# Kernel optimization log

Hardware: AMD Instinct MI355X
Metric: run time of the kernel (lower is better)

Reference implementation:

```python
import jax, jax.numpy as jnp
import numpy as np

U, I, G = 200000, 100000, 10000
D = 64
LAYERS = 3
E_HG = 3_000_000
E_GI = 2_000_000
B = 8192


def setup_inputs() -> dict:
    key = jax.random.key(0)
    ks = jax.random.split(key, 20)
    n_hg = U + G
    n_gi = G + I
    xav = lambda k, shape: (jax.random.normal(k, shape, jnp.float32) * 0.05)
    inp = {
        "user_inputs": jax.random.randint(ks[0], (B,), 0, U),
        "pos_groups": jax.random.randint(ks[1], (B,), 0, G),
        "neg_groups": jax.random.randint(ks[2], (B,), 0, G),
        # hypergraph propagation matrix (normalized-adjacency-like values)
        "hg_rows": jax.random.randint(ks[3], (E_HG,), 0, n_hg),
        "hg_cols": jax.random.randint(ks[4], (E_HG,), 0, n_hg),
        "hg_vals": jax.random.uniform(ks[5], (E_HG,), jnp.float32) / 16.0,
        # group-item bipartite graph (one LightGCN hop)
        "gi_rows": jax.random.randint(ks[6], (E_GI,), 0, n_gi),
        "gi_cols": jax.random.randint(ks[7], (E_GI,), 0, n_gi),
        "gi_vals": jax.random.uniform(ks[8], (E_GI,), jnp.float32) / 16.0,
        # dense group-group overlap matrix
        "gg_graph": jax.random.uniform(ks[9], (G, G), jnp.float32) / float(G),
        # learned parameters
        "user_emb": xav(ks[10], (U, D)),
        "item_emb": xav(ks[11], (I, D)),
        "group_emb": xav(ks[12], (G, D)),
        "hyper_w": xav(ks[13], (D, 1)),
        "hyper_b": jnp.zeros((1,), jnp.float32),
        "lightgcn_w": xav(ks[14], (D, 1)),
        "lightgcn_b": jnp.zeros((1,), jnp.float32),
        "overlap_w": xav(ks[15], (D, 1)),
        "overlap_b": jnp.zeros((1,), jnp.float32),
    }
    return inp


def spmm(rows, cols, vals, x, n):
    # sparse(n,n) @ x : gather cols, scale, scatter-add into rows
    return jax.ops.segment_sum(vals[:, None] * x[cols], rows, num_segments=n)


def reference(user_inputs, pos_groups, neg_groups,
              hg_rows, hg_cols, hg_vals,
              gi_rows, gi_cols, gi_vals,
              gg_graph,
              user_emb, item_emb, group_emb,
              hyper_w, hyper_b, lightgcn_w, lightgcn_b, overlap_w, overlap_b):
    # --- hypergraph branch: layered SpMM + mean over (layers+1) views ---
    hg = jnp.concatenate([user_emb, group_emb], axis=0)  # [U+G, D]
    acc = hg
    cur = hg
    for _ in range(LAYERS):
        cur = spmm(hg_rows, hg_cols, hg_vals, cur, U + G)
        acc = acc + cur
    hg_mean = acc / float(LAYERS + 1)
    hg_users = hg_mean[:U]   # [U, D]
    hg_groups = hg_mean[U:]  # [G, D]

    # --- lightgcn branch: one SpMM hop over group-item graph ---
    gi = jnp.concatenate([group_emb, item_emb], axis=0)  # [G+I, D]
    gi = spmm(gi_rows, gi_cols, gi_vals, gi, G + I)
    gi_groups = gi[:G]

    # --- overlap branch: dense group-group propagation ---
    gg = gg_graph @ group_emb  # [G, D]

    # --- gated multi-view fusion ---
    sig = jax.nn.sigmoid
    hyper_coef = sig(hg_groups @ hyper_w + hyper_b)      # [G, 1]
    lightgcn_coef = sig(gi_groups @ lightgcn_w + lightgcn_b)
    overlap_coef = sig(gg @ overlap_w + overlap_b)
    groups_final = hyper_coef * hg_groups + lightgcn_coef * gi_groups + overlap_coef * gg
    users_final = hg_users

    return (users_final[user_inputs], groups_final[pos_groups], groups_final[neg_groups],
            user_emb[user_inputs], group_emb[pos_groups], group_emb[neg_groups])
```

## Files before the change

### kernel.cpp

```cpp
#include <hip/hip_runtime.h>
#include <hip/hip_bf16.h>

#define U_N 200000
#define I_N 100000
#define G_N 10000
#define B_N 8192
#define NHG (U_N + G_N)
#define GG_K 10000
#define GG_KC 313
#define GG_STRIPES 157
#define GG_SPLIT 8

#define BUCK_SHIFT 8
#define BUCK_ROWS 256
#define NBUCK 821
#define ACHUNK 12288

typedef __attribute__((ext_vector_type(8))) short bf16x8;
typedef __attribute__((ext_vector_type(4))) float f32x4;

static __device__ __forceinline__ float sigmoidf_(float x) {
    return 1.0f / (1.0f + __expf(-x));
}

static __device__ __forceinline__ unsigned bfc(float x) {
    unsigned u = __float_as_uint(x);
    return (u + 0x7fffu + ((u >> 16) & 1u)) >> 16;
}
static __device__ __forceinline__ float blo(unsigned u) { return __uint_as_float(u << 16); }
static __device__ __forceinline__ float bhi(unsigned u) { return __uint_as_float(u & 0xffff0000u); }

__global__ void k_phase1(const float4* __restrict__ ue4, const float4* __restrict__ ge4,
                         ushort4* __restrict__ out4, const int* __restrict__ ui,
                         float* __restrict__ ua, float* __restrict__ grp_acc,
                         float* __restrict__ gi_out, short* __restrict__ Bfrag,
                         int* __restrict__ cursor, int cap,
                         int cvtB, int uaB, int gaB, int gzB, int bfB) {
    int bx = blockIdx.x;
    if (bx < cvtB) {
        int i = bx * 256 + threadIdx.x;
        float4 f = (i < U_N * 16) ? ue4[i] : ge4[i - U_N * 16];
        ushort4 o;
        o.x = (unsigned short)bfc(f.x);
        o.y = (unsigned short)bfc(f.y);
        o.z = (unsigned short)bfc(f.z);
        o.w = (unsigned short)bfc(f.w);
        out4[i] = o;
        return;
    }
    bx -= cvtB;
    if (bx < uaB) {
        int idx = bx * 256 + threadIdx.x;
        int b = idx >> 6, d = idx & 63;
        ua[idx] = ((const float*)ue4)[(size_t)ui[b] * 64 + d];
        return;
    }
    bx -= uaB;
    if (bx < gaB) {
        int idx = bx * 256 + threadIdx.x;
        grp_acc[idx] = ((const float*)ge4)[idx];
        return;
    }
    bx -= gaB;
    if (bx < gzB) {
        int idx = bx * 256 + threadIdx.x;
        gi_out[idx] = 0.f;
        return;
    }
    bx -= gzB;
    if (bx < bfB) {
        int t = bx * 256 + threadIdx.x;
        int l = t & 63;
        int ct = (t >> 6) & 3;
        int kc = t >> 8;
        int j = ct * 16 + (l & 15);
        int kb = kc * 32 + (l >> 4) * 8;
        bf16x8 pack;
#pragma unroll
        for (int e = 0; e < 8; ++e) {
            int k = kb + e;
            float f = (k < GG_K) ? ((const float*)ge4)[(size_t)k * 64 + j] : 0.f;
            pack[e] = (short)bfc(f);
        }
        *(bf16x8*)(Bfrag + (size_t)t * 8) = pack;
        return;
    }
    bx -= bfB;
    int b = bx * 256 + threadIdx.x;
    if (b < NBUCK) cursor[b] = b * cap;
}


static __device__ __forceinline__ void bscatter_body(const int* __restrict__ rows,
                                                     const int* __restrict__ cols,
                                                     const float* __restrict__ vals,
                                                     int* __restrict__ cursor,
                                                     int2* __restrict__ bpair,
                                                     int nE, int cap, int blk) {
    __shared__ int h[NBUCK];
    __shared__ int base[NBUCK];
    for (int i = threadIdx.x; i < NBUCK; i += 256) h[i] = 0;
    __syncthreads();
    int s = blk * ACHUNK;
    int end = s + ACHUNK; if (end > nE) end = nE;
    for (int e = s + threadIdx.x; e < end; e += 256)
        atomicAdd(&h[rows[e] >> BUCK_SHIFT], 1);
    __syncthreads();
    for (int i = threadIdx.x; i < NBUCK; i += 256) {
        int c = h[i];
        base[i] = c ? atomicAdd(&cursor[i], c) : 0;
        h[i] = 0;
    }
    __syncthreads();
    for (int e = s + threadIdx.x; e < end; e += 256) {
        int r = rows[e];
        int b = r >> BUCK_SHIFT;
        int pos = base[b] + atomicAdd(&h[b], 1);
        if (pos < (b + 1) * cap)
            bpair[pos] = make_int2(((r & (BUCK_ROWS - 1)) << 24) | cols[e],
                                   __float_as_int(vals[e]));
    }
}

static __device__ __forceinline__ void gg_mfma_body(const float* __restrict__ A,
                                                    const short* __restrict__ Bfrag,
                                                    float* __restrict__ part, int blk) {
    const int stripe = blk % GG_STRIPES;
    const int ks = blk / GG_STRIPES;
    const int w = threadIdx.x >> 6;
    const int l = threadIdx.x & 63;
    const int r0w = stripe * 64 + w * 16;
    int arow_i = r0w + (l & 15);
    if (arow_i > GG_K - 1) arow_i = GG_K - 1;
    const float* arow = A + (size_t)arow_i * GG_K;
    const int kg8 = (l >> 4) * 8;
    const int c0 = (ks == 0) ? 0 : 40 + 39 * (ks - 1);
    const int c1 = c0 + ((ks == 0) ? 40 : 39);
    f32x4 acc0 = {0.f, 0.f, 0.f, 0.f}, acc1 = acc0, acc2 = acc0, acc3 = acc0;
    for (int kc = c0; kc < c1; ++kc) {
        const int kbase = kc * 32 + kg8;
        bf16x8 af;
        if (kc != GG_KC - 1) {
            const float4 a0 = *(const float4*)(arow + kbase);
            const float4 a1 = *(const float4*)(arow + kbase + 4);
            af[0] = (short)bfc(a0.x); af[1] = (short)bfc(a0.y);
            af[2] = (short)bfc(a0.z); af[3] = (short)bfc(a0.w);
            af[4] = (short)bfc(a1.x); af[5] = (short)bfc(a1.y);
            af[6] = (short)bfc(a1.z); af[7] = (short)bfc(a1.w);
        } else {
#pragma unroll
            for (int e = 0; e < 8; ++e) {
                int k = kbase + e;
                af[e] = (short)bfc((k < GG_K) ? arow[k] : 0.f);
            }
        }
        const bf16x8* bp = (const bf16x8*)(Bfrag + (size_t)kc * 4 * 64 * 8);
        bf16x8 b0 = bp[0 * 64 + l];
        bf16x8 b1 = bp[1 * 64 + l];
        bf16x8 b2 = bp[2 * 64 + l];
        bf16x8 b3 = bp[3 * 64 + l];
        acc0 = __builtin_amdgcn_mfma_f32_16x16x32_bf16(af, b0, acc0, 0, 0, 0);
        acc1 = __builtin_amdgcn_mfma_f32_16x16x32_bf16(af, b1, acc1, 0, 0, 0);
        acc2 = __builtin_amdgcn_mfma_f32_16x16x32_bf16(af, b2, acc2, 0, 0, 0);
        acc3 = __builtin_amdgcn_mfma_f32_16x16x32_bf16(af, b3, acc3, 0, 0, 0);
    }
    float* po = part + (size_t)ks * GG_K * 64;
    const int orow0 = r0w + (l >> 4) * 4;
    const int ocol = l & 15;
#pragma unroll
    for (int reg = 0; reg < 4; ++reg) {
        int orow = orow0 + reg;
        if (orow < GG_K) {
            float* q = po + (size_t)orow * 64 + ocol;
            q[0]  = acc0[reg];
            q[16] = acc1[reg];
            q[32] = acc2[reg];
            q[48] = acc3[reg];
        }
    }
}

__global__ __launch_bounds__(256) void k_phase2(const int* __restrict__ rows,
                                                const int* __restrict__ cols,
                                                const float* __restrict__ vals,
                                                int* __restrict__ cursor,
                                                int2* __restrict__ bpair, int nE, int cap,
                                                const float* __restrict__ A,
                                                const short* __restrict__ Bfrag,
                                                float* __restrict__ part, int bsB) {
    if (blockIdx.x < bsB)
        bscatter_body(rows, cols, vals, cursor, bpair, nE, cap, blockIdx.x);
    else
        gg_mfma_body(A, Bfrag, part, blockIdx.x - bsB);
}


static __device__ __forceinline__ void bcsr_body(const int* __restrict__ cursor,
                                                 const int2* __restrict__ bpair,
                                                 int2* __restrict__ ep,
                                                 int* __restrict__ rp, int* __restrict__ cnt,
                                                 int cap, int b) {
    __shared__ int hist[256];
    __shared__ int sc[256];
    const int tid = threadIdx.x;
    const int s = b * cap;
    int e_ = cursor[b];
    if (e_ > s + cap) e_ = s + cap;
    hist[tid] = 0;
    __syncthreads();
    for (int i = s + tid; i < e_; i += 256)
        atomicAdd(&hist[((unsigned)bpair[i].x) >> 24], 1);
    __syncthreads();
    int v = hist[tid];
    sc[tid] = v;
    __syncthreads();
    for (int off = 1; off < 256; off <<= 1) {
        int t = (tid >= off) ? sc[tid - off] : 0;
        __syncthreads();
        if (tid >= off) sc[tid] += t;
        __syncthreads();
    }
    int excl = sc[tid] - v;
    int gr = (b << BUCK_SHIFT) + tid;
    if (gr < NHG) { rp[gr] = s + excl; cnt[gr] = v; }
    hist[tid] = excl;
    __syncthreads();
    for (int i = s + tid; i < e_; i += 256) {
        int2 p = bpair[i];
        unsigned pk = (unsigned)p.x;
        int pos = atomicAdd(&hist[pk >> 24], 1);
        ep[s + pos] = make_int2((int)(pk & 0xFFFFFFu), p.y);
    }
}

static __device__ __forceinline__ void gi_body(const int* __restrict__ rows,
                                               const int* __restrict__ cols,
                                               const float* __restrict__ vals,
                                               const float* __restrict__ ge,
                                               const float* __restrict__ ie,
                                               float* __restrict__ out, int nE,
                                               int blk, int nblk) {
    int lane = threadIdx.x & 63;
    long wslot = (long)blk * 4 + (threadIdx.x >> 6);
    const long nslots = (long)nblk * 4;
    for (long base = wslot * 64; base < nE; base += nslots * 64) {
        long e = base + lane;
        int r = (e < nE) ? rows[e] : 0x7fffffff;
        bool ok = (r < G_N);
        int c = 0;
        float v = 0.f;
        if (ok) { c = cols[e]; v = vals[e]; }
        unsigned long long mask = __ballot(ok);
        while (mask) {
            int srcl = __ffsll(mask) - 1;
            mask &= mask - 1;
            int rr = __shfl(r, srcl, 64);
            int cc = __shfl(c, srcl, 64);
            float vv = __shfl(v, srcl, 64);
            const float* sp = (cc < G_N) ? (ge + (size_t)cc * 64) : (ie + (size_t)(cc - G_N) * 64);
            atomicAdd(&out[(size_t)rr * 64 + lane], vv * sp[lane]);
        }
    }
}

__global__ __launch_bounds__(256) void k_phase3(const int* __restrict__ cursor,
                                                const int2* __restrict__ bpair,
                                                int2* __restrict__ ep,
                                                int* __restrict__ rp, int* __restrict__ cnt,
                                                int cap,
                                                const int* __restrict__ grows,
                                                const int* __restrict__ gcols,
                                                const float* __restrict__ gvals,
                                                const float* __restrict__ ge,
                                                const float* __restrict__ ie,
                                                float* __restrict__ gi_out, int gnE, int giB) {
    if (blockIdx.x < NBUCK)
        bcsr_body(cursor, bpair, ep, rp, cnt, cap, blockIdx.x);
    else
        gi_body(grows, gcols, gvals, ge, ie, gi_out, gnE, blockIdx.x - NBUCK, giB);
}


static __device__ __forceinline__ void spmm_row2(const int2* __restrict__ ep, int s, int n,
                                                 int nmax, const unsigned* __restrict__ x32,
                                                 int sub, float& ax, float& ay) {
    ax = 0.f; ay = 0.f;
    for (int i = 0; i < nmax; i += 8) {
        int2 e[8];
#pragma unroll
        for (int j = 0; j < 8; ++j) {
            int k = i + j;
            int kk = (k < n) ? k : (n > 0 ? n - 1 : 0);
            e[j] = ep[s + kk];
            if (k >= n) e[j].y = 0;
        }
        unsigned xv[8];
#pragma unroll
        for (int j = 0; j < 8; ++j)
            xv[j] = x32[(size_t)e[j].x * 32 + sub];
#pragma unroll
        for (int j = 0; j < 8; ++j) {
            float v = __int_as_float(e[j].y);
            ax += v * blo(xv[j]);
            ay += v * bhi(xv[j]);
        }
    }
}

__global__ void k_spmm2(const int* __restrict__ rp, const int* __restrict__ cnt,
                        const int2* __restrict__ ep, const unsigned* __restrict__ x32,
                        unsigned* __restrict__ out32, float* __restrict__ grp_acc,
                        const int* __restrict__ ui, float* __restrict__ usr_acc,
                        int spmmBlocks) {
    if (blockIdx.x >= spmmBlocks) {
        int idx = (blockIdx.x - spmmBlocks) * 256 + threadIdx.x;
        int b = idx >> 5, d = idx & 31;
        unsigned u = x32[(size_t)ui[b] * 32 + d];
        float2* g = (float2*)usr_acc + ((size_t)b * 32 + d);
        float2 t = *g;
        t.x += blo(u); t.y += bhi(u);
        *g = t;
        return;
    }
    int wid = threadIdx.x >> 6;
    int lane = threadIdx.x & 63;
    int half = lane >> 5, sub = lane & 31;
    int r = blockIdx.x * 8 + wid * 2 + half;
    bool active = (r < NHG);
    int rr = active ? r : NHG - 1;
    int s = rp[rr];
    int n = active ? cnt[rr] : 0;
    int nmax = n;
    nmax = max(nmax, __shfl_xor(nmax, 32, 64));
    float ax, ay;
    spmm_row2(ep, s, n, nmax, x32, sub, ax, ay);
    if (active) {
        out32[(size_t)r * 32 + sub] = bfc(ax) | (bfc(ay) << 16);
        if (r >= U_N) {
            float2* g = (float2*)grp_acc + ((size_t)(r - U_N) * 32 + sub);
            float2 t = *g;
            t.x += ax; t.y += ay;
            *g = t;
        }
    }
}

__global__ void k_spmm_final(const int* __restrict__ rp, const int* __restrict__ cnt,
                             const int2* __restrict__ ep, const unsigned* __restrict__ x32,
                             const int* __restrict__ ui,
                             float* __restrict__ grp_acc, float* __restrict__ usr_acc,
                             int taskBlocks) {
    if (blockIdx.x >= taskBlocks) {
        int idx = (blockIdx.x - taskBlocks) * 256 + threadIdx.x;
        int b = idx >> 5, d = idx & 31;
        unsigned u = x32[(size_t)ui[b] * 32 + d];
        float2* g = (float2*)usr_acc + ((size_t)b * 32 + d);
        float2 t = *g;
        t.x += blo(u); t.y += bhi(u);
        *g = t;
        return;
    }
    int wid = threadIdx.x >> 6;
    int lane = threadIdx.x & 63;
    int half = lane >> 5, sub = lane & 31;
    int t = blockIdx.x * 8 + wid * 2 + half;
    bool active = (t < G_N + B_N);
    int tt = active ? t : 0;
    int r = (tt < G_N) ? (U_N + tt) : ui[tt - G_N];
    int s = rp[r];
    int n = active ? cnt[r] : 0;
    int nmax = n;
    nmax = max(nmax, __shfl_xor(nmax, 32, 64));
    float ax, ay;
    spmm_row2(ep, s, n, nmax, x32, sub, ax, ay);
    if (active) {
        float2* g = (tt < G_N) ? ((float2*)grp_acc + ((size_t)tt * 32 + sub))
                               : ((float2*)usr_acc + ((size_t)(tt - G_N) * 32 + sub));
        float2 v = *g;
        v.x += ax; v.y += ay;
        *g = v;
    }
}


__global__ void k_finalize(const float* __restrict__ ga, const float* __restrict__ gi,
                           const float* __restrict__ gg_part, const float* __restrict__ hw,
                           const float* __restrict__ hb, const float* __restrict__ lw,
                           const float* __restrict__ lb, const float* __restrict__ ow,
                           const float* __restrict__ ob, float* __restrict__ gf) {
    int g = blockIdx.x * 4 + (threadIdx.x >> 6);
    if (g >= G_N) return;
    int lane = threadIdx.x & 63;
    size_t o = (size_t)g * 64 + lane;
    float hgv = ga[o] * 0.25f;
    float giv = gi[o];
    const size_t S = (size_t)GG_K * 64;
    float ggv = 0.f;
#pragma unroll
    for (int p = 0; p < GG_SPLIT; ++p) ggv += gg_part[p * S + o];
    float d1 = hgv * hw[lane], d2 = giv * lw[lane], d3 = ggv * ow[lane];
#pragma unroll
    for (int off = 32; off; off >>= 1) {
        d1 += __shfl_xor(d1, off, 64);
        d2 += __shfl_xor(d2, off, 64);
        d3 += __shfl_xor(d3, off, 64);
    }
    float hc = sigmoidf_(d1 + hb[0]);
    float lc = sigmoidf_(d2 + lb[0]);
    float oc = sigmoidf_(d3 + ob[0]);
    gf[o] = hc * hgv + lc * giv + oc * ggv;
}


__global__ void k_gather_out(const int* __restrict__ ui, const int* __restrict__ pg,
                             const int* __restrict__ ng, const float* __restrict__ ua,
                             const float* __restrict__ gf, const float* __restrict__ ue,
                             const float* __restrict__ ge, float* __restrict__ out) {
    int idx = blockIdx.x * 256 + threadIdx.x;
    if (idx >= B_N * 64) return;
    int b = idx >> 6, d = idx & 63;
    const int S = B_N * 64;
    int u = ui[b], p = pg[b], q = ng[b];
    out[idx]         = ua[idx] * 0.25f;
    out[S + idx]     = gf[(size_t)p * 64 + d];
    out[2 * S + idx] = gf[(size_t)q * 64 + d];
    out[3 * S + idx] = ue[(size_t)u * 64 + d];
    out[4 * S + idx] = ge[(size_t)p * 64 + d];
    out[5 * S + idx] = ge[(size_t)q * 64 + d];
}

extern "C" void kernel_launch(void* const* d_in, const int* in_sizes, int n_in,
                              void* d_out, int out_size, void* d_ws, size_t ws_size,
                              hipStream_t stream) {
    const int*   ui        = (const int*)d_in[0];
    const int*   pg        = (const int*)d_in[1];
    const int*   ng        = (const int*)d_in[2];
    const int*   hg_rows   = (const int*)d_in[3];
    const int*   hg_cols   = (const int*)d_in[4];
    const float* hg_vals   = (const float*)d_in[5];
    const int*   gi_rows   = (const int*)d_in[6];
    const int*   gi_cols   = (const int*)d_in[7];
    const float* gi_vals   = (const float*)d_in[8];
    const float* gg_graph  = (const float*)d_in[9];
    const float* user_emb  = (const float*)d_in[10];
    const float* item_emb  = (const float*)d_in[11];
    const float* group_emb = (const float*)d_in[12];
    const float* hyper_w   = (const float*)d_in[13];
    const float* hyper_b   = (const float*)d_in[14];
    const float* lgcn_w    = (const float*)d_in[15];
    const float* lgcn_b    = (const float*)d_in[16];
    const float* ovl_w     = (const float*)d_in[17];
    const float* ovl_b     = (const float*)d_in[18];
    const int E_HG = in_sizes[3];
    const int E_GI = in_sizes[6];

    const int nblkA = (E_HG + ACHUNK - 1) / ACHUNK;
    int cap = (E_HG + NBUCK - 1) / NBUCK;
    cap = cap + cap / 4 + 64;
    cap = (cap + 63) & ~63;

    char* ws = (char*)d_ws;
    size_t off = 0;
    auto alloc = [&](size_t bytes) -> char* {
        char* p = ws + off;
        off += (bytes + 255) & ~(size_t)255;
        return p;
    };
    int*   cursor  = (int*)alloc((size_t)NBUCK * 4);
    int2*  bpair   = (int2*)alloc((size_t)NBUCK * cap * 8);
    int2*  ep      = (int2*)alloc((size_t)NBUCK * cap * 8 + 1024);
    int*   rp      = (int*)alloc((size_t)NHG * 4);
    int*   cnt     = (int*)alloc((size_t)NHG * 4);
    __hip_bfloat16* curA = (__hip_bfloat16*)alloc((size_t)NHG * 64 * 2);
    __hip_bfloat16* curB = (__hip_bfloat16*)alloc((size_t)NHG * 64 * 2);
    float* grp_acc = (float*)alloc((size_t)G_N * 64 * 4);
    float* gi_out  = (float*)alloc((size_t)G_N * 64 * 4);
    float* grp_fin = (float*)alloc((size_t)G_N * 64 * 4);
    float* usr_acc = (float*)alloc((size_t)B_N * 64 * 4);
    short* Bfrag   = (short*)alloc((size_t)GG_KC * 4 * 64 * 8 * 2);
    float* gg_part = (float*)alloc((size_t)GG_SPLIT * GG_K * 64 * 4);
    (void)ws_size; (void)n_in; (void)out_size;

    const int cvtB = (NHG * 16) / 256;
    const int uaB  = (B_N * 64) / 256;
    const int gaB  = (G_N * 64) / 256;
    const int gzB  = (G_N * 64) / 256;
    const int bfB  = GG_KC;
    k_phase1<<<cvtB + uaB + gaB + gzB + bfB + 4, 256, 0, stream>>>(
        (const float4*)user_emb, (const float4*)group_emb, (ushort4*)curB, ui, usr_acc,
        grp_acc, gi_out, Bfrag, cursor, cap, cvtB, uaB, gaB, gzB, bfB);

    k_phase2<<<nblkA + GG_STRIPES * GG_SPLIT, 256, 0, stream>>>(
        hg_rows, hg_cols, hg_vals, cursor, bpair, E_HG, cap,
        gg_graph, Bfrag, gg_part, nblkA);

    const int giB = 2048;
    k_phase3<<<NBUCK + giB, 256, 0, stream>>>(cursor, bpair, ep, rp, cnt, cap,
                                              gi_rows, gi_cols, gi_vals,
                                              group_emb, item_emb, gi_out, E_GI, giB);

    const int spmmB = (NHG + 7) / 8;
    const int uaExt = (B_N * 32) / 256;

    k_spmm2<<<spmmB, 256, 0, stream>>>(rp, cnt, ep, (const unsigned*)curB,
                                       (unsigned*)curA, grp_acc, nullptr, nullptr, spmmB);
    k_spmm2<<<spmmB + uaExt, 256, 0, stream>>>(rp, cnt, ep, (const unsigned*)curA,
                                               (unsigned*)curB, grp_acc, ui, usr_acc, spmmB);
    const int taskB = (G_N + B_N + 7) / 8;
    k_spmm_final<<<taskB + uaExt, 256, 0, stream>>>(rp, cnt, ep, (const unsigned*)curB, ui,
                                                    grp_acc, usr_acc, taskB);

    k_finalize<<<(G_N + 3) / 4, 256, 0, stream>>>(grp_acc, gi_out, gg_part, hyper_w, hyper_b,
                                                  lgcn_w, lgcn_b, ovl_w, ovl_b, grp_fin);
    k_gather_out<<<(B_N * 64 + 255) / 256, 256, 0, stream>>>(ui, pg, ng, usr_acc, grp_fin,
                                                             user_emb, group_emb,
                                                             (float*)d_out);
}
```

Measured before the change: 472.0 us.

## Widen SpMM rows to 16 lanes, fuse finalize into gather, merge phase1 into phase2

The SpMM kernels now give each row 16 lanes that each load 8 bytes (four bf16 values), so a wave processes four rows instead of two. This cuts per-row lane overhead and raises memory-level parallelism. The gated group fusion is computed only for the sampled pos/neg groups inside the output gather kernel, which drops the full 10000-group finalize pass and the grp_fin buffer. The bf16 conversion and accumulator initialisation move from phase1 into the phase2 launch so they overlap with the bucket scatter and the GEMM. Fusing into the gather repeats the fusion work for groups that are sampled more than once.

Result: faster. 443.6 us (-6.0%).

```diff
diff --git a/kernel.cpp b/kernel.cpp
--- a/kernel.cpp
+++ b/kernel.cpp
@@ -29,45 +29,13 @@
 }
 static __device__ __forceinline__ float blo(unsigned u) { return __uint_as_float(u << 16); }
 static __device__ __forceinline__ float bhi(unsigned u) { return __uint_as_float(u & 0xffff0000u); }
-
-__global__ void k_phase1(const float4* __restrict__ ue4, const float4* __restrict__ ge4,
-                         ushort4* __restrict__ out4, const int* __restrict__ ui,
-                         float* __restrict__ ua, float* __restrict__ grp_acc,
-                         float* __restrict__ gi_out, short* __restrict__ Bfrag,
-                         int* __restrict__ cursor, int cap,
-                         int cvtB, int uaB, int gaB, int gzB, int bfB) {
+static __device__ __forceinline__ float bsf(unsigned short u) {
+    return __uint_as_float((unsigned)u << 16);
+}
+
+__global__ void k_phase1(const float* __restrict__ ge, short* __restrict__ Bfrag,
+                         int* __restrict__ cursor, int cap, int bfB) {
     int bx = blockIdx.x;
-    if (bx < cvtB) {
-        int i = bx * 256 + threadIdx.x;
-        float4 f = (i < U_N * 16) ? ue4[i] : ge4[i - U_N * 16];
-        ushort4 o;
-        o.x = (unsigned short)bfc(f.x);
-        o.y = (unsigned short)bfc(f.y);
-        o.z = (unsigned short)bfc(f.z);
-        o.w = (unsigned short)bfc(f.w);
-        out4[i] = o;
-        return;
-    }
-    bx -= cvtB;
-    if (bx < uaB) {
-        int idx = bx * 256 + threadIdx.x;
-        int b = idx >> 6, d = idx & 63;
-        ua[idx] = ((const float*)ue4)[(size_t)ui[b] * 64 + d];
-        return;
-    }
-    bx -= uaB;
-    if (bx < gaB) {
-        int idx = bx * 256 + threadIdx.x;
-        grp_acc[idx] = ((const float*)ge4)[idx];
-        return;
-    }
-    bx -= gaB;
-    if (bx < gzB) {
-        int idx = bx * 256 + threadIdx.x;
-        gi_out[idx] = 0.f;
-        return;
-    }
-    bx -= gzB;
     if (bx < bfB) {
         int t = bx * 256 + threadIdx.x;
         int l = t & 63;
@@ -79,14 +47,13 @@
 #pragma unroll
         for (int e = 0; e < 8; ++e) {
             int k = kb + e;
-            float f = (k < GG_K) ? ((const float*)ge4)[(size_t)k * 64 + j] : 0.f;
+            float f = (k < GG_K) ? ge[(size_t)k * 64 + j] : 0.f;
             pack[e] = (short)bfc(f);
         }
         *(bf16x8*)(Bfrag + (size_t)t * 8) = pack;
         return;
     }
-    bx -= bfB;
-    int b = bx * 256 + threadIdx.x;
+    int b = (bx - bfB) * 256 + threadIdx.x;
     if (b < NBUCK) cursor[b] = b * cap;
 }
 
@@ -180,18 +147,48 @@
     }
 }
 
-__global__ __launch_bounds__(256) void k_phase2(const int* __restrict__ rows,
-                                                const int* __restrict__ cols,
-                                                const float* __restrict__ vals,
-                                                int* __restrict__ cursor,
-                                                int2* __restrict__ bpair, int nE, int cap,
-                                                const float* __restrict__ A,
-                                                const short* __restrict__ Bfrag,
-                                                float* __restrict__ part, int bsB) {
-    if (blockIdx.x < bsB)
-        bscatter_body(rows, cols, vals, cursor, bpair, nE, cap, blockIdx.x);
-    else
-        gg_mfma_body(A, Bfrag, part, blockIdx.x - bsB);
+__global__ __launch_bounds__(256) void k_phase2(
+    const int* __restrict__ rows, const int* __restrict__ cols,
+    const float* __restrict__ vals, int* __restrict__ cursor,
+    int2* __restrict__ bpair, int nE, int cap,
+    const float* __restrict__ A, const short* __restrict__ Bfrag,
+    float* __restrict__ part,
+    const float4* __restrict__ ue4, const float4* __restrict__ ge4,
+    ushort4* __restrict__ out4, const int* __restrict__ ui,
+    float* __restrict__ ua, float* __restrict__ grp_acc, float* __restrict__ gi_out,
+    int bsB, int ggB, int cvtB, int uaB, int gaB) {
+    int bx = blockIdx.x;
+    if (bx < bsB) { bscatter_body(rows, cols, vals, cursor, bpair, nE, cap, bx); return; }
+    bx -= bsB;
+    if (bx < ggB) { gg_mfma_body(A, Bfrag, part, bx); return; }
+    bx -= ggB;
+    if (bx < cvtB) {
+        int i = bx * 256 + threadIdx.x;
+        float4 f = (i < U_N * 16) ? ue4[i] : ge4[i - U_N * 16];
+        ushort4 o;
+        o.x = (unsigned short)bfc(f.x);
+        o.y = (unsigned short)bfc(f.y);
+        o.z = (unsigned short)bfc(f.z);
+        o.w = (unsigned short)bfc(f.w);
+        out4[i] = o;
+        return;
+    }
+    bx -= cvtB;
+    if (bx < uaB) {
+        int idx = bx * 256 + threadIdx.x;
+        int b = idx >> 6, d = idx & 63;
+        ua[idx] = ((const float*)ue4)[(size_t)ui[b] * 64 + d];
+        return;
+    }
+    bx -= uaB;
+    if (bx < gaB) {
+        int idx = bx * 256 + threadIdx.x;
+        grp_acc[idx] = ((const float*)ge4)[idx];
+        return;
+    }
+    bx -= gaB;
+    int idx = bx * 256 + threadIdx.x;
+    gi_out[idx] = 0.f;
 }
 
 
@@ -281,10 +278,10 @@
 }
 
 
-static __device__ __forceinline__ void spmm_row2(const int2* __restrict__ ep, int s, int n,
-                                                 int nmax, const unsigned* __restrict__ x32,
-                                                 int sub, float& ax, float& ay) {
-    ax = 0.f; ay = 0.f;
+static __device__ __forceinline__ void spmm_row4(const int2* __restrict__ ep, int s, int n,
+                                                 int nmax, const ushort4* __restrict__ x8,
+                                                 int sub, float4& acc) {
+    acc.x = 0.f; acc.y = 0.f; acc.z = 0.f; acc.w = 0.f;
     for (int i = 0; i < nmax; i += 8) {
         int2 e[8];
 #pragma unroll
@@ -292,141 +289,144 @@
             int k = i + j;
             int kk = (k < n) ? k : (n > 0 ? n - 1 : 0);
             e[j] = ep[s + kk];
-            if (k >= n) e[j].y = 0;
-        }
-        unsigned xv[8];
+            if (k >= n) { e[j].y = 0; e[j].x = 0; }
+        }
+        ushort4 xv[8];
 #pragma unroll
         for (int j = 0; j < 8; ++j)
-            xv[j] = x32[(size_t)e[j].x * 32 + sub];
+            xv[j] = x8[(size_t)e[j].x * 16 + sub];
 #pragma unroll
         for (int j = 0; j < 8; ++j) {
             float v = __int_as_float(e[j].y);
-            ax += v * blo(xv[j]);
-            ay += v * bhi(xv[j]);
-        }
-    }
-}
-
-__global__ void k_spmm2(const int* __restrict__ rp, const int* __restrict__ cnt,
-                        const int2* __restrict__ ep, const unsigned* __restrict__ x32,
-                        unsigned* __restrict__ out32, float* __restrict__ grp_acc,
+            acc.x += v * bsf(xv[j].x);
+            acc.y += v * bsf(xv[j].y);
+            acc.z += v * bsf(xv[j].z);
+            acc.w += v * bsf(xv[j].w);
+        }
+    }
+}
+
+static __device__ __forceinline__ int slotmax(int n) {
+    int m = max(n, __shfl_xor(n, 16, 64));
+    return max(m, __shfl_xor(m, 32, 64));
+}
+
+__global__ void k_spmm4(const int* __restrict__ rp, const int* __restrict__ cnt,
+                        const int2* __restrict__ ep, const ushort4* __restrict__ x8,
+                        ushort4* __restrict__ out8, float* __restrict__ grp_acc,
                         const int* __restrict__ ui, float* __restrict__ usr_acc,
                         int spmmBlocks) {
     if (blockIdx.x >= spmmBlocks) {
         int idx = (blockIdx.x - spmmBlocks) * 256 + threadIdx.x;
-        int b = idx >> 5, d = idx & 31;
-        unsigned u = x32[(size_t)ui[b] * 32 + d];
-        float2* g = (float2*)usr_acc + ((size_t)b * 32 + d);
-        float2 t = *g;
-        t.x += blo(u); t.y += bhi(u);
+        int b = idx >> 4, d = idx & 15;
+        ushort4 u = x8[(size_t)ui[b] * 16 + d];
+        float4* g = (float4*)usr_acc + ((size_t)b * 16 + d);
+        float4 t = *g;
+        t.x += bsf(u.x); t.y += bsf(u.y); t.z += bsf(u.z); t.w += bsf(u.w);
         *g = t;
         return;
     }
     int wid = threadIdx.x >> 6;
     int lane = threadIdx.x & 63;
-    int half = lane >> 5, sub = lane & 31;
-    int r = blockIdx.x * 8 + wid * 2 + half;
-    bool active = (r < NHG);
-    int rr = active ? r : NHG - 1;
-    int s = rp[rr];
-    int n = active ? cnt[rr] : 0;
-    int nmax = n;
-    nmax = max(nmax, __shfl_xor(nmax, 32, 64));
-    float ax, ay;
-    spmm_row2(ep, s, n, nmax, x32, sub, ax, ay);
-    if (active) {
-        out32[(size_t)r * 32 + sub] = bfc(ax) | (bfc(ay) << 16);
-        if (r >= U_N) {
-            float2* g = (float2*)grp_acc + ((size_t)(r - U_N) * 32 + sub);
-            float2 t = *g;
-            t.x += ax; t.y += ay;
-            *g = t;
-        }
-    }
-}
-
-__global__ void k_spmm_final(const int* __restrict__ rp, const int* __restrict__ cnt,
-                             const int2* __restrict__ ep, const unsigned* __restrict__ x32,
-                             const int* __restrict__ ui,
-                             float* __restrict__ grp_acc, float* __restrict__ usr_acc,
-                             int taskBlocks) {
+    int slot = lane >> 4, sub = lane & 15;
+    int r = blockIdx.x * 16 + wid * 4 + slot;
+    int s = rp[r];
+    int n = cnt[r];
+    int nmax = slotmax(n);
+    float4 a;
+    spmm_row4(ep, s, n, nmax, x8, sub, a);
+    ushort4 o;
+    o.x = (unsigned short)bfc(a.x);
+    o.y = (unsigned short)bfc(a.y);
+    o.z = (unsigned short)bfc(a.z);
+    o.w = (unsigned short)bfc(a.w);
+    out8[(size_t)r * 16 + sub] = o;
+    if (r >= U_N) {
+        float4* g = (float4*)grp_acc + ((size_t)(r - U_N) * 16 + sub);
+        float4 t = *g;
+        t.x += a.x; t.y += a.y; t.z += a.z; t.w += a.w;
+        *g = t;
+    }
+}
+
+__global__ void k_spmm4_final(const int* __restrict__ rp, const int* __restrict__ cnt,
+                              const int2* __restrict__ ep, const ushort4* __restrict__ x8,
+                              const int* __restrict__ ui,
+                              float* __restrict__ grp_acc, float* __restrict__ usr_acc,
+                              int taskBlocks) {
     if (blockIdx.x >= taskBlocks) {
         int idx = (blockIdx.x - taskBlocks) * 256 + threadIdx.x;
-        int b = idx >> 5, d = idx & 31;
-        unsigned u = x32[(size_t)ui[b] * 32 + d];
-        float2* g = (float2*)usr_acc + ((size_t)b * 32 + d);
-        float2 t = *g;
-        t.x += blo(u); t.y += bhi(u);
+        int b = idx >> 4, d = idx & 15;
+        ushort4 u = x8[(size_t)ui[b] * 16 + d];
+        float4* g = (float4*)usr_acc + ((size_t)b * 16 + d);
+        float4 t = *g;
+        t.x += bsf(u.x); t.y += bsf(u.y); t.z += bsf(u.z); t.w += bsf(u.w);
         *g = t;
         return;
     }
     int wid = threadIdx.x >> 6;
     int lane = threadIdx.x & 63;
-    int half = lane >> 5, sub = lane & 31;
-    int t = blockIdx.x * 8 + wid * 2 + half;
+    int slot = lane >> 4, sub = lane & 15;
+    int t = blockIdx.x * 16 + wid * 4 + slot;
     bool active = (t < G_N + B_N);
     int tt = active ? t : 0;
     int r = (tt < G_N) ? (U_N + tt) : ui[tt - G_N];
     int s = rp[r];
     int n = active ? cnt[r] : 0;
-    int nmax = n;
-    nmax = max(nmax, __shfl_xor(nmax, 32, 64));
-    float ax, ay;
-    spmm_row2(ep, s, n, nmax, x32, sub, ax, ay);
+    int nmax = slotmax(n);
+    float4 a;
+    spmm_row4(ep, s, n, nmax, x8, sub, a);
     if (active) {
-        float2* g = (tt < G_N) ? ((float2*)grp_acc + ((size_t)tt * 32 + sub))
-                               : ((float2*)usr_acc + ((size_t)(tt - G_N) * 32 + sub));
-        float2 v = *g;
-        v.x += ax; v.y += ay;
+        float4* g = (tt < G_N) ? ((float4*)grp_acc + ((size_t)tt * 16 + sub))
+                               : ((float4*)usr_acc + ((size_t)(tt - G_N) * 16 + sub));
+        float4 v = *g;
+        v.x += a.x; v.y += a.y; v.z += a.z; v.w += a.w;
         *g = v;
     }
 }
 
 
-__global__ void k_finalize(const float* __restrict__ ga, const float* __restrict__ gi,
-                           const float* __restrict__ gg_part, const float* __restrict__ hw,
-                           const float* __restrict__ hb, const float* __restrict__ lw,
-                           const float* __restrict__ lb, const float* __restrict__ ow,
-                           const float* __restrict__ ob, float* __restrict__ gf) {
-    int g = blockIdx.x * 4 + (threadIdx.x >> 6);
-    if (g >= G_N) return;
-    int lane = threadIdx.x & 63;
-    size_t o = (size_t)g * 64 + lane;
-    float hgv = ga[o] * 0.25f;
-    float giv = gi[o];
-    const size_t S = (size_t)GG_K * 64;
-    float ggv = 0.f;
-#pragma unroll
-    for (int p = 0; p < GG_SPLIT; ++p) ggv += gg_part[p * S + o];
-    float d1 = hgv * hw[lane], d2 = giv * lw[lane], d3 = ggv * ow[lane];
-#pragma unroll
-    for (int off = 32; off; off >>= 1) {
-        d1 += __shfl_xor(d1, off, 64);
-        d2 += __shfl_xor(d2, off, 64);
-        d3 += __shfl_xor(d3, off, 64);
-    }
-    float hc = sigmoidf_(d1 + hb[0]);
-    float lc = sigmoidf_(d2 + lb[0]);
-    float oc = sigmoidf_(d3 + ob[0]);
-    gf[o] = hc * hgv + lc * giv + oc * ggv;
-}
-
-
-__global__ void k_gather_out(const int* __restrict__ ui, const int* __restrict__ pg,
+__global__ void k_gather_fin(const int* __restrict__ ui, const int* __restrict__ pg,
                              const int* __restrict__ ng, const float* __restrict__ ua,
-                             const float* __restrict__ gf, const float* __restrict__ ue,
-                             const float* __restrict__ ge, float* __restrict__ out) {
-    int idx = blockIdx.x * 256 + threadIdx.x;
-    if (idx >= B_N * 64) return;
-    int b = idx >> 6, d = idx & 63;
+                             const float* __restrict__ ga, const float* __restrict__ gi_out,
+                             const float* __restrict__ gg_part,
+                             const float* __restrict__ hw, const float* __restrict__ hb,
+                             const float* __restrict__ lw, const float* __restrict__ lb,
+                             const float* __restrict__ ow, const float* __restrict__ ob,
+                             const float* __restrict__ ue, const float* __restrict__ ge,
+                             float* __restrict__ out) {
+    int wid = threadIdx.x >> 6, lane = threadIdx.x & 63;
+    int b = blockIdx.x * 4 + wid;
     const int S = B_N * 64;
     int u = ui[b], p = pg[b], q = ng[b];
+    int idx = b * 64 + lane;
     out[idx]         = ua[idx] * 0.25f;
-    out[S + idx]     = gf[(size_t)p * 64 + d];
-    out[2 * S + idx] = gf[(size_t)q * 64 + d];
-    out[3 * S + idx] = ue[(size_t)u * 64 + d];
-    out[4 * S + idx] = ge[(size_t)p * 64 + d];
-    out[5 * S + idx] = ge[(size_t)q * 64 + d];
+    out[3 * S + idx] = ue[(size_t)u * 64 + lane];
+    out[4 * S + idx] = ge[(size_t)p * 64 + lane];
+    out[5 * S + idx] = ge[(size_t)q * 64 + lane];
+    const size_t SS = (size_t)G_N * 64;
+    float hwv = hw[lane], lwv = lw[lane], owv = ow[lane];
+    float hb0 = hb[0], lb0 = lb[0], ob0 = ob[0];
+#pragma unroll
+    for (int which = 0; which < 2; ++which) {
+        int g = which ? q : p;
+        size_t o = (size_t)g * 64 + lane;
+        float hgv = ga[o] * 0.25f;
+        float giv = gi_out[o];
+        float ggv = 0.f;
+#pragma unroll
+        for (int k = 0; k < GG_SPLIT; ++k) ggv += gg_part[k * SS + o];
+        float d1 = hgv * hwv, d2 = giv * lwv, d3 = ggv * owv;
+#pragma unroll
+        for (int off2 = 32; off2; off2 >>= 1) {
+            d1 += __shfl_xor(d1, off2, 64);
+            d2 += __shfl_xor(d2, off2, 64);
+            d3 += __shfl_xor(d3, off2, 64);
+        }
+        float val = sigmoidf_(d1 + hb0) * hgv + sigmoidf_(d2 + lb0) * giv
+                  + sigmoidf_(d3 + ob0) * ggv;
+        out[(which ? 2 * S : S) + idx] = val;
+    }
 }
 
 extern "C" void kernel_launch(void* const* d_in, const int* in_sizes, int n_in,
@@ -475,44 +475,41 @@
     __hip_bfloat16* curB = (__hip_bfloat16*)alloc((size_t)NHG * 64 * 2);
     float* grp_acc = (float*)alloc((size_t)G_N * 64 * 4);
     float* gi_out  = (float*)alloc((size_t)G_N * 64 * 4);
-    float* grp_fin = (float*)alloc((size_t)G_N * 64 * 4);
     float* usr_acc = (float*)alloc((size_t)B_N * 64 * 4);
     short* Bfrag   = (short*)alloc((size_t)GG_KC * 4 * 64 * 8 * 2);
     float* gg_part = (float*)alloc((size_t)GG_SPLIT * GG_K * 64 * 4);
     (void)ws_size; (void)n_in; (void)out_size;
 
+    k_phase1<<<GG_KC + 4, 256, 0, stream>>>(group_emb, Bfrag, cursor, cap, GG_KC);
+
+    const int ggB  = GG_STRIPES * GG_SPLIT;
     const int cvtB = (NHG * 16) / 256;
     const int uaB  = (B_N * 64) / 256;
     const int gaB  = (G_N * 64) / 256;
     const int gzB  = (G_N * 64) / 256;
-    const int bfB  = GG_KC;
-    k_phase1<<<cvtB + uaB + gaB + gzB + bfB + 4, 256, 0, stream>>>(
-        (const float4*)user_emb, (const float4*)group_emb, (ushort4*)curB, ui, usr_acc,
-        grp_acc, gi_out, Bfrag, cursor, cap, cvtB, uaB, gaB, gzB, bfB);
-
-    k_phase2<<<nblkA + GG_STRIPES * GG_SPLIT, 256, 0, stream>>>(
+    k_phase2<<<nblkA + ggB + cvtB + uaB + gaB + gzB, 256, 0, stream>>>(
         hg_rows, hg_cols, hg_vals, cursor, bpair, E_HG, cap,
-        gg_graph, Bfrag, gg_part, nblkA);
+        gg_graph, Bfrag, gg_part,
+        (const float4*)user_emb, (const float4*)group_emb, (ushort4*)curB, ui,
+        usr_acc, grp_acc, gi_out, nblkA, ggB, cvtB, uaB, gaB);
 
     const int giB = 2048;
     k_phase3<<<NBUCK + giB, 256, 0, stream>>>(cursor, bpair, ep, rp, cnt, cap,
                                               gi_rows, gi_cols, gi_vals,
                                               group_emb, item_emb, gi_out, E_GI, giB);
 
-    const int spmmB = (NHG + 7) / 8;
-    const int uaExt = (B_N * 32) / 256;
-
-    k_spmm2<<<spmmB, 256, 0, stream>>>(rp, cnt, ep, (const unsigned*)curB,
-                                       (unsigned*)curA, grp_acc, nullptr, nullptr, spmmB);
-    k_spmm2<<<spmmB + uaExt, 256, 0, stream>>>(rp, cnt, ep, (const unsigned*)curA,
-                                               (unsigned*)curB, grp_acc, ui, usr_acc, spmmB);
-    const int taskB = (G_N + B_N + 7) / 8;
-    k_spmm_final<<<taskB + uaExt, 256, 0, stream>>>(rp, cnt, ep, (const unsigned*)curB, ui,
-                                                    grp_acc, usr_acc, taskB);
-
-    k_finalize<<<(G_N + 3) / 4, 256, 0, stream>>>(grp_acc, gi_out, gg_part, hyper_w, hyper_b,
-                                                  lgcn_w, lgcn_b, ovl_w, ovl_b, grp_fin);
-    k_gather_out<<<(B_N * 64 + 255) / 256, 256, 0, stream>>>(ui, pg, ng, usr_acc, grp_fin,
-                                                             user_emb, group_emb,
-                                                             (float*)d_out);
-}
+    const int spmmB = NHG / 16;
+    const int uaExt = (B_N * 16) / 256;
+
+    k_spmm4<<<spmmB, 256, 0, stream>>>(rp, cnt, ep, (const ushort4*)curB,
+                                       (ushort4*)curA, grp_acc, nullptr, nullptr, spmmB);
+    k_spmm4<<<spmmB + uaExt, 256, 0, stream>>>(rp, cnt, ep, (const ushort4*)curA,
+                                               (ushort4*)curB, grp_acc, ui, usr_acc, spmmB);
+    const int taskB = (G_N + B_N + 15) / 16;
+    k_spmm4_final<<<taskB + uaExt, 256, 0, stream>>>(rp, cnt, ep, (const ushort4*)curB, ui,
+                                                     grp_acc, usr_acc, taskB);
+
+    k_gather_fin<<<B_N / 4, 256, 0, stream>>>(ui, pg, ng, usr_acc, grp_acc, gi_out, gg_part,
+                                              hyper_w, hyper_b, lgcn_w, lgcn_b, ovl_w, ovl_b,
+                                              user_emb, group_emb, (float*)d_out);
+}
```
